# Kernel optimization log

Measured on AMD Instinct MI355X. Metric: run time of the kernel, lower is better.

Reference implementation:

```python
import jax, jax.numpy as jnp
import numpy as np

D = 128          # fine voxel grid resolution
N0 = 250000
D_IN, D_BASE, D_OUT = 16, 8, 8
EPS = 1e-5
# (cin, cout) for conv0..conv6, conv7, conv9, conv11
_CH = [(16, 8), (8, 16), (16, 16), (16, 32), (32, 32), (32, 64), (64, 64), (64, 32), (32, 16), (16, 8)]

def _offsets():
    r = np.arange(-1, 2)
    return np.stack(np.meshgrid(r, r, r, indexing='ij'), -1).reshape(-1, 3)  # [27,3]

def _lookup_fn(coords, d):
    keys = (coords[:, 0].astype(np.int64) * d + coords[:, 1]) * d + coords[:, 2]
    order = np.argsort(keys)
    skeys = keys[order]
    def lookup(q):
        valid = ((q >= 0) & (q < d)).all(-1)
        k = (q[:, 0].astype(np.int64) * d + q[:, 1]) * d + q[:, 2]
        pos = np.clip(np.searchsorted(skeys, k), 0, len(skeys) - 1)
        return np.where(valid & (skeys[pos] == k), order[pos], -1).astype(np.int32)
    return lookup

def _nbr_same(coords, d):
    # stride-1 sparse conv: outputs at input coords, neighbors at coord+k
    lk = _lookup_fn(coords, d)
    return np.stack([lk(coords + o) for o in _offsets()], 1)  # [N,27]

def _nbr_down(c_out, c_in, d_in):
    # stride-2 conv: output p gathers inputs at 2p+k
    lk = _lookup_fn(c_in, d_in)
    return np.stack([lk(c_out * 2 + o) for o in _offsets()], 1)

def _nbr_up(c_out, c_in, d_in):
    # transposed stride-2 conv: output q gathers input p=(q-k)/2 where divisible
    lk = _lookup_fn(c_in, d_in)
    cols = []
    for o in _offsets():
        q = c_out - o
        div = (q % 2 == 0).all(-1)
        cols.append(np.where(div, lk(q // 2), -1).astype(np.int32))
    return np.stack(cols, 1)

def setup_inputs():
    rng = np.random.default_rng(0)
    flat = rng.choice(D ** 3, size=N0, replace=False)
    c0 = np.stack([flat // (D * D), (flat // D) % D, flat % D], 1).astype(np.int32)
    c1 = np.unique(c0 // 2, axis=0)
    c2 = np.unique(c1 // 2, axis=0)
    c3 = np.unique(c2 // 2, axis=0)
    inp = {
        'feats': jax.random.normal(jax.random.key(0), (N0, D_IN), jnp.float32),
        'nbr0': jnp.asarray(_nbr_same(c0, D)),
        'nbr_d01': jnp.asarray(_nbr_down(c1, c0, D)),
        'nbr1': jnp.asarray(_nbr_same(c1, D // 2)),
        'nbr_d12': jnp.asarray(_nbr_down(c2, c1, D // 2)),
        'nbr2': jnp.asarray(_nbr_same(c2, D // 4)),
        'nbr_d23': jnp.asarray(_nbr_down(c3, c2, D // 4)),
        'nbr3': jnp.asarray(_nbr_same(c3, D // 8)),
        'nbr_u32': jnp.asarray(_nbr_up(c2, c3, D // 8)),
        'nbr_u21': jnp.asarray(_nbr_up(c1, c2, D // 4)),
        'nbr_u10': jnp.asarray(_nbr_up(c0, c1, D // 2)),
    }
    key = jax.random.key(1)
    for i, (ci, co) in enumerate(_CH):
        key, kw = jax.random.split(key)
        inp['w%d' % i] = jax.random.normal(kw, (27, ci, co), jnp.float32) / np.sqrt(27.0 * ci)
        inp['g%d' % i] = jnp.ones((co,), jnp.float32)
        inp['b%d' % i] = jnp.zeros((co,), jnp.float32)
    inp['lin_w'] = jax.random.normal(jax.random.key(2), (D_OUT, D_BASE), jnp.float32) / np.sqrt(D_BASE)
    return inp

def _sconv_bn_relu(f, nbr, w, g, b):
    # f: [Nin,Cin], nbr: [Nout,27] (-1 = no neighbor), w: [27,Cin,Cout]
    gth = jnp.where((nbr >= 0)[..., None], f[jnp.maximum(nbr, 0)], 0.0)  # [Nout,27,Cin]
    y = jnp.einsum('nkc,kco->no', gth, w)
    mu = y.mean(0)                       # training-mode BatchNorm over active voxels
    var = y.var(0)
    return jax.nn.relu((y - mu) * jax.lax.rsqrt(var + EPS) * g + b)

def reference(feats, nbr0, nbr_d01, nbr1, nbr_d12, nbr2, nbr_d23, nbr3, nbr_u32, nbr_u21, nbr_u10,
              w0, g0, b0, w1, g1, b1, w2, g2, b2, w3, g3, b3, w4, g4, b4,
              w5, g5, b5, w6, g6, b6, w7, g7, b7, w8, g8, b8, w9, g9, b9, lin_w):
    c0f = _sconv_bn_relu(feats, nbr0, w0, g0, b0)
    c2f = _sconv_bn_relu(_sconv_bn_relu(c0f, nbr_d01, w1, g1, b1), nbr1, w2, g2, b2)
    c4f = _sconv_bn_relu(_sconv_bn_relu(c2f, nbr_d12, w3, g3, b3), nbr2, w4, g4, b4)
    x = _sconv_bn_relu(_sconv_bn_relu(c4f, nbr_d23, w5, g5, b5), nbr3, w6, g6, b6)
    x = c4f + _sconv_bn_relu(x, nbr_u32, w7, g7, b7)
    x = c2f + _sconv_bn_relu(x, nbr_u21, w8, g8, b8)
    x = c0f + _sconv_bn_relu(x, nbr_u10, w9, g9, b9)
    return x @ lin_w.T, x
```

## Files before the change

### kernel.cpp

```cpp
#include <hip/hip_runtime.h>

#define EPSV 1e-5f
#define NBUCKET 64

typedef __attribute__((ext_vector_type(8))) short short8;
typedef __attribute__((ext_vector_type(4))) float float4v;

static inline int cdiv(int a, int b) { return (a + b - 1) / b; }
static inline int imin(int a, int b) { return a < b ? a : b; }

__device__ inline unsigned short f2bf(float x) {
  unsigned u = __float_as_uint(x);
  return (unsigned short)((u + 0x7FFFu + ((u >> 16) & 1u)) >> 16);
}
__device__ inline float bf2f(unsigned short u) {
  return __uint_as_float(((unsigned)u) << 16);
}

struct PrepArgs {
  const float* w[10];
  unsigned short* wt[10];
  int ci[10];
  int co[10];
  int wcum[11];
  const float* feats;
  unsigned short* featsb;
  int nfeat4;
  float* stats;
};

__global__ __launch_bounds__(256) void prep_kernel(PrepArgs p, long total) {
  const int nstat4 = 10 * NBUCKET * 128 / 4;
  for (long tid0 = (long)blockIdx.x * 256 + threadIdx.x; tid0 < total;
       tid0 += (long)gridDim.x * 256) {
    long tid = tid0;
    if (tid < nstat4) {
      ((float4*)p.stats)[tid] = make_float4(0.f, 0.f, 0.f, 0.f);
      continue;
    }
    tid -= nstat4;
    if (tid < p.nfeat4) {
      float4 v = ((const float4*)p.feats)[tid];
      ushort4 r;
      r.x = f2bf(v.x); r.y = f2bf(v.y); r.z = f2bf(v.z); r.w = f2bf(v.w);
      ((ushort4*)p.featsb)[tid] = r;
      continue;
    }
    tid -= p.nfeat4;
    if (tid >= p.wcum[10]) continue;
    int i = 0;
    while (tid >= p.wcum[i + 1]) ++i;
    int e = (int)(tid - p.wcum[i]);
    int ci = p.ci[i], co = p.co[i];
    int k = e / (ci * co);
    int r = e - k * (ci * co);
    int o = r / ci;
    int c = r - o * ci;
    p.wt[i][((long)k * co + o) * ci + c] = f2bf(p.w[i][((long)k * ci + c) * co + o]);
  }
}

template<int CI, int CO, int MINW>
__global__ __launch_bounds__(256, MINW) void conv_mfma(
    const unsigned short* __restrict__ f, const int* __restrict__ nbr,
    const unsigned short* __restrict__ wt, unsigned short* __restrict__ y,
    float* __restrict__ stats, int nout) {
  constexpr int NCHUNK = (CI == 8) ? 7 : (CI == 16) ? 14 : (CI == 32) ? 27 : 54;
  constexpr int CIP = (CI == 64) ? 64 : (CI == 32) ? 40 : (CI == 16) ? 24 : 12;
  constexpr int RB = (CO < 16) ? CO : 16;

  __shared__ int nbrT[64 * 27];
  __shared__ unsigned short Bs[27 * RB * CIP];

  const int tid = threadIdx.x;
  const int lane = tid & 63;
  const int wid = tid >> 6;
  const int m = lane & 15;
  const int mm = m & (RB - 1);
  const int quad = lane >> 4;
  const int cbase = blockIdx.y * 16;
  const int co = cbase + m;
  const bool cok = co < CO;

  auto tapof = [&](int c) -> int {
    if constexpr (CI == 8) return c * 4 + quad;
    else if constexpr (CI == 16) return c * 2 + (quad >> 1);
    else if constexpr (CI == 32) return c;
    else return c >> 1;
  };
  auto cioof = [&](int c) -> int {
    if constexpr (CI == 8) return 0;
    else if constexpr (CI == 16) return (quad & 1) * 8;
    else if constexpr (CI == 32) return quad * 8;
    else return ((c & 1) << 5) + quad * 8;
  };
  auto baddr = [&](int tap, int r, int cio) -> int {
    if constexpr (CI == 64) {
      int byt = (tap * 16 + r) * 128 + cio * 2;
      byt ^= (r & 7) << 4;
      return byt >> 1;
    } else {
      return (tap * RB + r) * CIP + cio;
    }
  };

  const int tile = blockIdx.x;
  const int rowb0 = tile * 64;

  {
    constexpr int NC8 = CI / 8;
    for (int t = tid; t < 27 * RB * NC8; t += 256) {
      int tap = t / (RB * NC8);
      int r = t - tap * (RB * NC8);
      int mo = r / NC8;
      int c8 = (r - mo * NC8) * 8;
      short8 v;
#pragma unroll
      for (int q = 0; q < 8; ++q) v[q] = 0;
      int c = cbase + mo;
      if (c < CO) v = *(const short8*)(wt + ((long)tap * CO + c) * CI + c8);
      *(short8*)&Bs[baddr(tap, mo, c8)] = v;
    }
  }
  {
    const long base = (long)rowb0 * 27;
    const long lim = (long)nout * 27;
    for (int j = tid; j < 432; j += 256) {
      long g = base + j * 4;
      int4 v;
      if (g + 4 <= lim) {
        v = *(const int4*)(nbr + g);
      } else {
        v.x = (g + 0 < lim) ? nbr[g + 0] : -1;
        v.y = (g + 1 < lim) ? nbr[g + 1] : -1;
        v.z = (g + 2 < lim) ? nbr[g + 2] : -1;
        v.w = (g + 3 < lim) ? nbr[g + 3] : -1;
      }
      *(int4*)&nbrT[j * 4] = v;
    }
  }
  __syncthreads();

  const int rowb = rowb0 + wid * 16;
  const int lrow = (wid * 16 + m) * 27;
  float4v acc = {0.f, 0.f, 0.f, 0.f};

  if constexpr (CI <= 16) {
    int idxs[NCHUNK];
#pragma unroll
    for (int c = 0; c < NCHUNK; ++c) {
      int tap = tapof(c);
      idxs[c] = (tap < 27) ? nbrT[lrow + tap] : -1;
    }
    short8 A[NCHUNK];
#pragma unroll
    for (int c = 0; c < NCHUNK; ++c) {
      short8 a;
#pragma unroll
      for (int q = 0; q < 8; ++q) a[q] = 0;
      if (idxs[c] >= 0) a = *(const short8*)(f + (long)idxs[c] * CI + cioof(c));
      A[c] = a;
    }
#pragma unroll
    for (int c = 0; c < NCHUNK; ++c) {
      int tap = tapof(c);
      int tapc = tap < 27 ? tap : 26;
      short8 bf = *(const short8*)&Bs[baddr(tapc, mm, cioof(c))];
      acc = __builtin_amdgcn_mfma_f32_16x16x32_bf16(A[c], bf, acc, 0, 0, 0);
    }
  } else {
    constexpr int G = 9;
    constexpr int NG = NCHUNK / G;
    short8 A[2][G];
    auto load_group = [&](int g, int bi) {
#pragma unroll
      for (int j = 0; j < G; ++j) {
        const int c = g * G + j;
        const int tap = tapof(c);
        int idx = nbrT[lrow + tap];
        short8 a;
#pragma unroll
        for (int q = 0; q < 8; ++q) a[q] = 0;
        if (idx >= 0) a = *(const short8*)(f + (long)idx * CI + cioof(c));
        A[bi][j] = a;
      }
    };
    load_group(0, 0);
#pragma unroll
    for (int g = 0; g < NG; ++g) {
      const int cur = g & 1;
      if (g + 1 < NG) load_group(g + 1, cur ^ 1);
#pragma unroll
      for (int j = 0; j < G; ++j) {
        const int c = g * G + j;
        short8 bf = *(const short8*)&Bs[baddr(tapof(c), mm, cioof(c))];
        acc = __builtin_amdgcn_mfma_f32_16x16x32_bf16(A[cur][j], bf, acc, 0, 0, 0);
      }
    }
  }

  float sum = 0.f, sq = 0.f;
#pragma unroll
  for (int r = 0; r < 4; ++r) {
    float v = acc[r];
    int orow = rowb + quad * 4 + r;
    if (cok && orow < nout) y[(long)orow * CO + co] = f2bf(v);
    sum += v;
    sq = fmaf(v, v, sq);
  }

  sum += __shfl_xor(sum, 16); sq += __shfl_xor(sq, 16);
  sum += __shfl_xor(sum, 32); sq += __shfl_xor(sq, 32);
  if (quad == 0 && cok) {
    float* st = stats + ((((unsigned)blockIdx.x * 4 + wid) & (NBUCKET - 1)) << 7);
    atomicAdd(&st[co], sum);
    atomicAdd(&st[64 + co], sq);
  }
}

template<int CO>
__global__ __launch_bounds__(256) void bn_relu_bf16(
    const unsigned short* __restrict__ y, const float* __restrict__ stats,
    const float* __restrict__ g, const float* __restrict__ b,
    const unsigned short* __restrict__ skip, unsigned short* __restrict__ out,
    int nout, float inv_n) {
  __shared__ float sA[CO], sC[CO];
  if ((int)threadIdx.x < CO) {
    int o = threadIdx.x;
    float su = 0.f, sq = 0.f;
#pragma unroll 8
    for (int bk = 0; bk < NBUCKET; ++bk) {
      su += stats[bk * 128 + o];
      sq += stats[bk * 128 + 64 + o];
    }
    float mu = su * inv_n;
    float var = sq * inv_n - mu * mu;
    float a = g[o] * rsqrtf(var + EPSV);
    sA[o] = a;
    sC[o] = fmaf(-mu, a, b[o]);
  }
  __syncthreads();
  long total4 = (long)nout * CO / 4;
  for (long i4 = (long)blockIdx.x * 256 + threadIdx.x; i4 < total4;
       i4 += (long)gridDim.x * 256) {
    int o = (int)((i4 * 4) % CO);
    ushort4 v = ((const ushort4*)y)[i4];
    float vv[4] = {bf2f(v.x), bf2f(v.y), bf2f(v.z), bf2f(v.w)};
    unsigned short rr[4];
#pragma unroll
    for (int j = 0; j < 4; ++j) {
      float x = fmaxf(fmaf(vv[j], sA[o + j], sC[o + j]), 0.f);
      if (skip) x += bf2f(skip[i4 * 4 + j]);
      rr[j] = f2bf(x);
    }
    ushort4 r;
    r.x = rr[0]; r.y = rr[1]; r.z = rr[2]; r.w = rr[3];
    ((ushort4*)out)[i4] = r;
  }
}

__global__ __launch_bounds__(256) void tail_kernel(
    const unsigned short* __restrict__ c0f, const float* __restrict__ st9,
    const float* __restrict__ g9, const float* __restrict__ b9, float inv_n,
    const float* __restrict__ lin_w, const unsigned short* __restrict__ y9,
    float* __restrict__ out0, float* __restrict__ x0, int n0) {
  __shared__ float swl[64];
  __shared__ float sbn[16];
  if (threadIdx.x < 64) swl[threadIdx.x] = lin_w[threadIdx.x];
  if (threadIdx.x < 8) {
    int o = threadIdx.x;
    float su = 0.f, sq = 0.f;
#pragma unroll 8
    for (int bk = 0; bk < NBUCKET; ++bk) {
      su += st9[bk * 128 + o];
      sq += st9[bk * 128 + 64 + o];
    }
    float mu = su * inv_n;
    float var = sq * inv_n - mu * mu;
    float a = g9[o] * rsqrtf(var + EPSV);
    sbn[o] = a;
    sbn[8 + o] = fmaf(-mu, a, b9[o]);
  }
  __syncthreads();
  for (int n = blockIdx.x * 256 + (int)threadIdx.x; n < n0; n += gridDim.x * 256) {
    const ushort4* pr = (const ushort4*)(y9 + (long)n * 8);
    ushort4 r0 = pr[0], r1 = pr[1];
    unsigned short rw[8] = {r0.x, r0.y, r0.z, r0.w, r1.x, r1.y, r1.z, r1.w};
    const ushort4* pc = (const ushort4*)(c0f + (long)n * 8);
    ushort4 c0 = pc[0], c1 = pc[1];
    unsigned short cs[8] = {c0.x, c0.y, c0.z, c0.w, c1.x, c1.y, c1.z, c1.w};
    float xv[8];
#pragma unroll
    for (int c = 0; c < 8; ++c)
      xv[c] = bf2f(cs[c]) + fmaxf(fmaf(bf2f(rw[c]), sbn[c], sbn[8 + c]), 0.f);
    *(float4*)(x0 + (long)n * 8) = make_float4(xv[0], xv[1], xv[2], xv[3]);
    *(float4*)(x0 + (long)n * 8 + 4) = make_float4(xv[4], xv[5], xv[6], xv[7]);
    float ov[8];
#pragma unroll
    for (int j = 0; j < 8; ++j) {
      float s = 0.f;
#pragma unroll
      for (int c = 0; c < 8; ++c) s = fmaf(xv[c], swl[j * 8 + c], s);
      ov[j] = s;
    }
    *(float4*)(out0 + (long)n * 8) = make_float4(ov[0], ov[1], ov[2], ov[3]);
    *(float4*)(out0 + (long)n * 8 + 4) = make_float4(ov[4], ov[5], ov[6], ov[7]);
  }
}

extern "C" void kernel_launch(void* const* d_in, const int* in_sizes, int n_in,
                              void* d_out, int out_size, void* d_ws, size_t ws_size,
                              hipStream_t stream) {
  const float* feats   = (const float*)d_in[0];
  const int* nbr0      = (const int*)d_in[1];
  const int* nbr_d01   = (const int*)d_in[2];
  const int* nbr1      = (const int*)d_in[3];
  const int* nbr_d12   = (const int*)d_in[4];
  const int* nbr2      = (const int*)d_in[5];
  const int* nbr_d23   = (const int*)d_in[6];
  const int* nbr3      = (const int*)d_in[7];
  const int* nbr_u32   = (const int*)d_in[8];
  const int* nbr_u21   = (const int*)d_in[9];
  const int* nbr_u10   = (const int*)d_in[10];
  const float* w[10];
  const float* g[10];
  const float* b[10];
  for (int i = 0; i < 10; ++i) {
    w[i] = (const float*)d_in[11 + 3 * i];
    g[i] = (const float*)d_in[12 + 3 * i];
    b[i] = (const float*)d_in[13 + 3 * i];
  }
  const float* lin_w = (const float*)d_in[41];

  const int N0 = in_sizes[0] / 16;
  const int N1 = in_sizes[2] / 27;
  const int N2 = in_sizes[4] / 27;
  const int N3 = in_sizes[6] / 27;
  const float i0 = 1.f / N0, i1 = 1.f / N1, i2 = 1.f / N2, i3 = 1.f / N3;

  static const int CIv[10] = {16, 8, 16, 16, 32, 32, 64, 64, 32, 16};
  static const int COv[10] = {8, 16, 16, 32, 32, 64, 64, 32, 16, 8};

  float* stats = (float*)d_ws;
  unsigned short* u = (unsigned short*)(stats + 10 * NBUCKET * 128);

  unsigned short* yraw = u; u += (size_t)N1 * 32;

  unsigned short* wt[10];
  int wcum[11];
  wcum[0] = 0;
  for (int i = 0; i < 10; ++i) {
    wt[i] = u;
    int sz = 27 * CIv[i] * COv[i];
    u += sz;
    wcum[i + 1] = wcum[i] + sz;
  }
  unsigned short* featsb = u; u += (size_t)N0 * 16;
  unsigned short* c0f = u;    u += (size_t)N0 * 8;
  unsigned short* t1  = u;    u += (size_t)N1 * 16;
  unsigned short* c2f = u;    u += (size_t)N1 * 16;
  unsigned short* t2  = u;    u += (size_t)N2 * 32;
  unsigned short* c4f = u;    u += (size_t)N2 * 32;
  unsigned short* t3  = u;    u += (size_t)N3 * 64;
  unsigned short* t4  = u;    u += (size_t)N3 * 64;
  unsigned short* t5  = t2;
  unsigned short* t6  = t1;
  float* out0 = (float*)d_out;
  float* x0   = (float*)d_out + (size_t)N0 * 8;

  float* s[10];
  for (int i = 0; i < 10; ++i) s[i] = stats + i * NBUCKET * 128;

  PrepArgs pa;
  for (int i = 0; i < 10; ++i) {
    pa.w[i] = w[i]; pa.wt[i] = wt[i];
    pa.ci[i] = CIv[i]; pa.co[i] = COv[i];
    pa.wcum[i] = wcum[i];
  }
  pa.wcum[10] = wcum[10];
  pa.feats = feats; pa.featsb = featsb;
  pa.nfeat4 = N0 * 16 / 4;
  pa.stats = stats;
  long prep_total = (10 * NBUCKET * 128 / 4) + pa.nfeat4 + wcum[10];
  prep_kernel<<<imin((int)((prep_total + 255) / 256), 2048), 256, 0, stream>>>(pa, prep_total);

  auto bgrid = [](long nout, int co) {
    return imin((int)((nout * co / 4 + 255) / 256), 1024);
  };

  int tb0 = cdiv(N0, 64), tb1 = cdiv(N1, 64), tb2 = cdiv(N2, 64), tb3 = cdiv(N3, 64);

  conv_mfma<16, 8, 6><<<dim3(tb0, 1), 256, 0, stream>>>(featsb, nbr0, wt[0], yraw, s[0], N0);
  bn_relu_bf16<8><<<bgrid(N0, 8), 256, 0, stream>>>(yraw, s[0], g[0], b[0], nullptr, c0f, N0, i0);

  conv_mfma<8, 16, 6><<<dim3(tb1, 1), 256, 0, stream>>>(c0f, nbr_d01, wt[1], yraw, s[1], N1);
  bn_relu_bf16<16><<<bgrid(N1, 16), 256, 0, stream>>>(yraw, s[1], g[1], b[1], nullptr, t1, N1, i1);

  conv_mfma<16, 16, 5><<<dim3(tb1, 1), 256, 0, stream>>>(t1, nbr1, wt[2], yraw, s[2], N1);
  bn_relu_bf16<16><<<bgrid(N1, 16), 256, 0, stream>>>(yraw, s[2], g[2], b[2], nullptr, c2f, N1, i1);

  conv_mfma<16, 32, 5><<<dim3(tb2, 2), 256, 0, stream>>>(c2f, nbr_d12, wt[3], yraw, s[3], N2);
  bn_relu_bf16<32><<<bgrid(N2, 32), 256, 0, stream>>>(yraw, s[3], g[3], b[3], nullptr, t2, N2, i2);

  conv_mfma<32, 32, 3><<<dim3(tb2, 2), 256, 0, stream>>>(t2, nbr2, wt[4], yraw, s[4], N2);
  bn_relu_bf16<32><<<bgrid(N2, 32), 256, 0, stream>>>(yraw, s[4], g[4], b[4], nullptr, c4f, N2, i2);

  conv_mfma<32, 64, 3><<<dim3(tb3, 4), 256, 0, stream>>>(c4f, nbr_d23, wt[5], yraw, s[5], N3);
  bn_relu_bf16<64><<<bgrid(N3, 64), 256, 0, stream>>>(yraw, s[5], g[5], b[5], nullptr, t3, N3, i3);

  conv_mfma<64, 64, 2><<<dim3(tb3, 4), 256, 0, stream>>>(t3, nbr3, wt[6], yraw, s[6], N3);
  bn_relu_bf16<64><<<bgrid(N3, 64), 256, 0, stream>>>(yraw, s[6], g[6], b[6], nullptr, t4, N3, i3);

  conv_mfma<64, 32, 2><<<dim3(tb2, 2), 256, 0, stream>>>(t4, nbr_u32, wt[7], yraw, s[7], N2);
  bn_relu_bf16<32><<<bgrid(N2, 32), 256, 0, stream>>>(yraw, s[7], g[7], b[7], c4f, t5, N2, i2);

  conv_mfma<32, 16, 3><<<dim3(tb1, 1), 256, 0, stream>>>(t5, nbr_u21, wt[8], yraw, s[8], N1);
  bn_relu_bf16<16><<<bgrid(N1, 16), 256, 0, stream>>>(yraw, s[8], g[8], b[8], c2f, t6, N1, i1);

  conv_mfma<16, 8, 6><<<dim3(tb0, 1), 256, 0, stream>>>(t6, nbr_u10, wt[9], yraw, s[9], N0);

  tail_kernel<<<imin(cdiv(N0, 256), 1024), 256, 0, stream>>>(
      c0f, s[9], g[9], b[9], i0, lin_w, yraw, out0, x0, N0);
}
```

Measured before the change: 428.2 us.

## Process two row tiles per block for small-CI convs and batch CI=32 gathers

For convolutions with CI<=16, each block now covers 128 output rows, two 64-row tiles. Each wave issues the gathers for both tiles before a scheduling barrier and then runs interleaved MFMAs that share each B fragment. For CI=32 the grouped double-buffer is replaced by issuing all 27 gathers up front, followed by 27 MFMAs. Launch bounds are lowered to 2-4 waves per SIMD to make room for the extra registers. This aims to expose more memory-level parallelism and amortize the weight staging in LDS, at the cost of fewer resident waves and half as many blocks.

```diff
diff --git a/kernel.cpp b/kernel.cpp
--- a/kernel.cpp
+++ b/kernel.cpp
@@ -68,8 +68,10 @@
   constexpr int NCHUNK = (CI == 8) ? 7 : (CI == 16) ? 14 : (CI == 32) ? 27 : 54;
   constexpr int CIP = (CI == 64) ? 64 : (CI == 32) ? 40 : (CI == 16) ? 24 : 12;
   constexpr int RB = (CO < 16) ? CO : 16;
-
-  __shared__ int nbrT[64 * 27];
+  constexpr bool TWO = (CI <= 16);
+  constexpr int NT = TWO ? 2 : 1;
+
+  __shared__ int nbrT[NT * 64 * 27];
   __shared__ unsigned short Bs[27 * RB * CIP];
 
   const int tid = threadIdx.x;
@@ -104,8 +106,7 @@
     }
   };
 
-  const int tile = blockIdx.x;
-  const int rowb0 = tile * 64;
+  const int rowb0 = blockIdx.x * (NT * 64);
 
   {
     constexpr int NC8 = CI / 8;
@@ -125,7 +126,7 @@
   {
     const long base = (long)rowb0 * 27;
     const long lim = (long)nout * 27;
-    for (int j = tid; j < 432; j += 256) {
+    for (int j = tid; j < NT * 432; j += 256) {
       long g = base + j * 4;
       int4 v;
       if (g + 4 <= lim) {
@@ -143,30 +144,84 @@
 
   const int rowb = rowb0 + wid * 16;
   const int lrow = (wid * 16 + m) * 27;
-  float4v acc = {0.f, 0.f, 0.f, 0.f};
-
-  if constexpr (CI <= 16) {
-    int idxs[NCHUNK];
+  float sum = 0.f, sq = 0.f;
+
+  if constexpr (TWO) {
+    int idx0[NCHUNK], idx1[NCHUNK];
 #pragma unroll
     for (int c = 0; c < NCHUNK; ++c) {
       int tap = tapof(c);
-      idxs[c] = (tap < 27) ? nbrT[lrow + tap] : -1;
-    }
-    short8 A[NCHUNK];
+      idx0[c] = (tap < 27) ? nbrT[lrow + tap] : -1;
+      idx1[c] = (tap < 27) ? nbrT[1728 + lrow + tap] : -1;
+    }
+    short8 A0[NCHUNK], A1[NCHUNK];
 #pragma unroll
     for (int c = 0; c < NCHUNK; ++c) {
       short8 a;
 #pragma unroll
       for (int q = 0; q < 8; ++q) a[q] = 0;
-      if (idxs[c] >= 0) a = *(const short8*)(f + (long)idxs[c] * CI + cioof(c));
-      A[c] = a;
-    }
+      if (idx0[c] >= 0) a = *(const short8*)(f + (long)idx0[c] * CI + cioof(c));
+      A0[c] = a;
+    }
+#pragma unroll
+    for (int c = 0; c < NCHUNK; ++c) {
+      short8 a;
+#pragma unroll
+      for (int q = 0; q < 8; ++q) a[q] = 0;
+      if (idx1[c] >= 0) a = *(const short8*)(f + (long)idx1[c] * CI + cioof(c));
+      A1[c] = a;
+    }
+    __builtin_amdgcn_sched_barrier(0);
+    float4v acc0 = {0.f, 0.f, 0.f, 0.f};
+    float4v acc1 = {0.f, 0.f, 0.f, 0.f};
 #pragma unroll
     for (int c = 0; c < NCHUNK; ++c) {
       int tap = tapof(c);
       int tapc = tap < 27 ? tap : 26;
       short8 bf = *(const short8*)&Bs[baddr(tapc, mm, cioof(c))];
+      acc0 = __builtin_amdgcn_mfma_f32_16x16x32_bf16(A0[c], bf, acc0, 0, 0, 0);
+      acc1 = __builtin_amdgcn_mfma_f32_16x16x32_bf16(A1[c], bf, acc1, 0, 0, 0);
+    }
+#pragma unroll
+    for (int r = 0; r < 4; ++r) {
+      float v0 = acc0[r];
+      int o0 = rowb + quad * 4 + r;
+      if (cok && o0 < nout) y[(long)o0 * CO + co] = f2bf(v0);
+      sum += v0;
+      sq = fmaf(v0, v0, sq);
+      float v1 = acc1[r];
+      int o1 = rowb + 64 + quad * 4 + r;
+      if (cok && o1 < nout) y[(long)o1 * CO + co] = f2bf(v1);
+      sum += v1;
+      sq = fmaf(v1, v1, sq);
+    }
+  } else if constexpr (CI == 32) {
+    int idxs[27];
+#pragma unroll
+    for (int t = 0; t < 27; ++t) idxs[t] = nbrT[lrow + t];
+    short8 A[27];
+#pragma unroll
+    for (int c = 0; c < 27; ++c) {
+      short8 a;
+#pragma unroll
+      for (int q = 0; q < 8; ++q) a[q] = 0;
+      if (idxs[c] >= 0) a = *(const short8*)(f + (long)idxs[c] * 32 + quad * 8);
+      A[c] = a;
+    }
+    __builtin_amdgcn_sched_barrier(0);
+    float4v acc = {0.f, 0.f, 0.f, 0.f};
+#pragma unroll
+    for (int c = 0; c < 27; ++c) {
+      short8 bf = *(const short8*)&Bs[baddr(c, mm, quad * 8)];
       acc = __builtin_amdgcn_mfma_f32_16x16x32_bf16(A[c], bf, acc, 0, 0, 0);
+    }
+#pragma unroll
+    for (int r = 0; r < 4; ++r) {
+      float v = acc[r];
+      int orow = rowb + quad * 4 + r;
+      if (cok && orow < nout) y[(long)orow * CO + co] = f2bf(v);
+      sum += v;
+      sq = fmaf(v, v, sq);
     }
   } else {
     constexpr int G = 9;
@@ -185,6 +240,7 @@
         A[bi][j] = a;
       }
     };
+    float4v acc = {0.f, 0.f, 0.f, 0.f};
     load_group(0, 0);
 #pragma unroll
     for (int g = 0; g < NG; ++g) {
@@ -197,16 +253,14 @@
         acc = __builtin_amdgcn_mfma_f32_16x16x32_bf16(A[cur][j], bf, acc, 0, 0, 0);
       }
     }
-  }
-
-  float sum = 0.f, sq = 0.f;
-#pragma unroll
-  for (int r = 0; r < 4; ++r) {
-    float v = acc[r];
-    int orow = rowb + quad * 4 + r;
-    if (cok && orow < nout) y[(long)orow * CO + co] = f2bf(v);
-    sum += v;
-    sq = fmaf(v, v, sq);
+#pragma unroll
+    for (int r = 0; r < 4; ++r) {
+      float v = acc[r];
+      int orow = rowb + quad * 4 + r;
+      if (cok && orow < nout) y[(long)orow * CO + co] = f2bf(v);
+      sum += v;
+      sq = fmaf(v, v, sq);
+    }
   }
 
   sum += __shfl_xor(sum, 16); sq += __shfl_xor(sq, 16);
@@ -388,36 +442,37 @@
     return imin((int)((nout * co / 4 + 255) / 256), 1024);
   };
 
-  int tb0 = cdiv(N0, 64), tb1 = cdiv(N1, 64), tb2 = cdiv(N2, 64), tb3 = cdiv(N3, 64);
-
-  conv_mfma<16, 8, 6><<<dim3(tb0, 1), 256, 0, stream>>>(featsb, nbr0, wt[0], yraw, s[0], N0);
+  int g2_0 = cdiv(N0, 128), g2_1 = cdiv(N1, 128), g2_2 = cdiv(N2, 128);
+  int g1_1 = cdiv(N1, 64), g1_2 = cdiv(N2, 64), g1_3 = cdiv(N3, 64);
+
+  conv_mfma<16, 8, 2><<<dim3(g2_0, 1), 256, 0, stream>>>(featsb, nbr0, wt[0], yraw, s[0], N0);
   bn_relu_bf16<8><<<bgrid(N0, 8), 256, 0, stream>>>(yraw, s[0], g[0], b[0], nullptr, c0f, N0, i0);
 
-  conv_mfma<8, 16, 6><<<dim3(tb1, 1), 256, 0, stream>>>(c0f, nbr_d01, wt[1], yraw, s[1], N1);
+  conv_mfma<8, 16, 4><<<dim3(g2_1, 1), 256, 0, stream>>>(c0f, nbr_d01, wt[1], yraw, s[1], N1);
   bn_relu_bf16<16><<<bgrid(N1, 16), 256, 0, stream>>>(yraw, s[1], g[1], b[1], nullptr, t1, N1, i1);
 
-  conv_mfma<16, 16, 5><<<dim3(tb1, 1), 256, 0, stream>>>(t1, nbr1, wt[2], yraw, s[2], N1);
+  conv_mfma<16, 16, 2><<<dim3(g2_1, 1), 256, 0, stream>>>(t1, nbr1, wt[2], yraw, s[2], N1);
   bn_relu_bf16<16><<<bgrid(N1, 16), 256, 0, stream>>>(yraw, s[2], g[2], b[2], nullptr, c2f, N1, i1);
 
-  conv_mfma<16, 32, 5><<<dim3(tb2, 2), 256, 0, stream>>>(c2f, nbr_d12, wt[3], yraw, s[3], N2);
+  conv_mfma<16, 32, 2><<<dim3(g2_2, 2), 256, 0, stream>>>(c2f, nbr_d12, wt[3], yraw, s[3], N2);
   bn_relu_bf16<32><<<bgrid(N2, 32), 256, 0, stream>>>(yraw, s[3], g[3], b[3], nullptr, t2, N2, i2);
 
-  conv_mfma<32, 32, 3><<<dim3(tb2, 2), 256, 0, stream>>>(t2, nbr2, wt[4], yraw, s[4], N2);
+  conv_mfma<32, 32, 2><<<dim3(g1_2, 2), 256, 0, stream>>>(t2, nbr2, wt[4], yraw, s[4], N2);
   bn_relu_bf16<32><<<bgrid(N2, 32), 256, 0, stream>>>(yraw, s[4], g[4], b[4], nullptr, c4f, N2, i2);
 
-  conv_mfma<32, 64, 3><<<dim3(tb3, 4), 256, 0, stream>>>(c4f, nbr_d23, wt[5], yraw, s[5], N3);
+  conv_mfma<32, 64, 2><<<dim3(g1_3, 4), 256, 0, stream>>>(c4f, nbr_d23, wt[5], yraw, s[5], N3);
   bn_relu_bf16<64><<<bgrid(N3, 64), 256, 0, stream>>>(yraw, s[5], g[5], b[5], nullptr, t3, N3, i3);
 
-  conv_mfma<64, 64, 2><<<dim3(tb3, 4), 256, 0, stream>>>(t3, nbr3, wt[6], yraw, s[6], N3);
+  conv_mfma<64, 64, 2><<<dim3(g1_3, 4), 256, 0, stream>>>(t3, nbr3, wt[6], yraw, s[6], N3);
   bn_relu_bf16<64><<<bgrid(N3, 64), 256, 0, stream>>>(yraw, s[6], g[6], b[6], nullptr, t4, N3, i3);
 
-  conv_mfma<64, 32, 2><<<dim3(tb2, 2), 256, 0, stream>>>(t4, nbr_u32, wt[7], yraw, s[7], N2);
+  conv_mfma<64, 32, 2><<<dim3(g1_2, 2), 256, 0, stream>>>(t4, nbr_u32, wt[7], yraw, s[7], N2);
   bn_relu_bf16<32><<<bgrid(N2, 32), 256, 0, stream>>>(yraw, s[7], g[7], b[7], c4f, t5, N2, i2);
 
-  conv_mfma<32, 16, 3><<<dim3(tb1, 1), 256, 0, stream>>>(t5, nbr_u21, wt[8], yraw, s[8], N1);
+  conv_mfma<32, 16, 2><<<dim3(g1_1, 1), 256, 0, stream>>>(t5, nbr_u21, wt[8], yraw, s[8], N1);
   bn_relu_bf16<16><<<bgrid(N1, 16), 256, 0, stream>>>(yraw, s[8], g[8], b[8], c2f, t6, N1, i1);
 
-  conv_mfma<16, 8, 6><<<dim3(tb0, 1), 256, 0, stream>>>(t6, nbr_u10, wt[9], yraw, s[9], N0);
+  conv_mfma<16, 8, 2><<<dim3(g2_0, 1), 256, 0, stream>>>(t6, nbr_u10, wt[9], yraw, s[9], N0);
 
   tail_kernel<<<imin(cdiv(N0, 256), 1024), 256, 0, stream>>>(
       c0f, s[9], g[9], b[9], i0, lin_w, yraw, out0, x0, N0);
```

Result: no change. 426.7 us (-0.4%).
